# Optimization experiments

Measured on AMD Instinct MI355X. Metric: run time of the kernel, lower is better.

Reference implementation:

```python
import jax, jax.numpy as jnp
import numpy as np

N, E, De, Dv = 40000, 8000, 32, 8   # nodes, hyperedges, edge degree, node degree
D, Q, EIG, VOC, NC = 256, 256, 64, 1000, 40  # vertex/edge dim, query dim, eig dim, centrality vocab, classes
LN_EPS = 1e-5


def _linear(x, W, b):
    return x @ W + b


def _layernorm(x, g, b):
    mu = jnp.mean(x, axis=-1, keepdims=True)
    var = jnp.mean(jnp.square(x - mu), axis=-1, keepdims=True)
    return (x - mu) * jax.lax.rsqrt(var + LN_EPS) * g + b


def setup_inputs() -> dict:
    key = jax.random.key(0)
    ks = iter(jax.random.split(key, 64))
    def nrm(shape, s=0.02):
        return (jax.random.normal(next(ks), shape, jnp.float32) * s).astype(jnp.float32)
    inp = {
        'vfeat': jax.random.normal(next(ks), (N, D), jnp.float32),
        'efeat': jax.random.normal(next(ks), (E, D), jnp.float32),
        'eign_vec': jax.random.normal(next(ks), (N, EIG), jnp.float32),
        'feat_v_gcn': jax.random.normal(next(ks), (N, D), jnp.float32),
        'cent1': jax.random.uniform(next(ks), (E, De), jnp.float32),
        'cent2': jax.random.uniform(next(ks), (N, Dv), jnp.float32),
        'cent_idx': jax.random.randint(next(ks), (N,), 0, VOC),
        'uniq_idx': jax.random.randint(next(ks), (N,), 0, VOC),
        'edge2node': jax.random.randint(next(ks), (E, De), 0, N),
        'node2edge': jax.random.randint(next(ks), (N, Dv), 0, E),
        # learned parameters (W: [in, out])
        'W_vtx': nrm((D, D)), 'b_vtx': jnp.zeros((D,), jnp.float32),
        'W_pe': nrm((EIG, D)), 'b_pe': jnp.zeros((D,), jnp.float32),
        'cs_emb': nrm((VOC, D)), 'un_emb': nrm((VOC, D)),
        'W_kv': nrm((D, Q)), 'b_kv': jnp.zeros((Q,), jnp.float32),
        'W_vv': nrm((D, D)), 'b_vv': jnp.zeros((D,), jnp.float32),
        'W_qe': nrm((D, Q)), 'b_qe': jnp.zeros((Q,), jnp.float32),
        'W_ke': nrm((D, Q)), 'b_ke': jnp.zeros((Q,), jnp.float32),
        'W_ve': nrm((D, D)), 'b_ve': jnp.zeros((D,), jnp.float32),
        'W_qv': nrm((D, Q)), 'b_qv': jnp.zeros((Q,), jnp.float32),
        'W_l1': nrm((D, Q)), 'b_l1': jnp.zeros((Q,), jnp.float32),
        'W_l2': nrm((Q, D)), 'b_l2': jnp.zeros((D,), jnp.float32),
        'W_l3': nrm((D, Q)), 'b_l3': jnp.zeros((Q,), jnp.float32),
        'W_l4': nrm((Q, D)), 'b_l4': jnp.zeros((D,), jnp.float32),
        'ln1_g': jnp.ones((D,), jnp.float32), 'ln1_b': jnp.zeros((D,), jnp.float32),
        'ln2_g': jnp.ones((D,), jnp.float32), 'ln2_b': jnp.zeros((D,), jnp.float32),
        'W_cls': nrm((D, NC)), 'b_cls': jnp.zeros((NC,), jnp.float32),
    }
    return inp


def _forward(vfeat, efeat, eign_vec, feat_v_gcn, cent1, cent2,
             W_vtx, b_vtx, W_pe, b_pe, cs_emb, un_emb,
             W_kv, b_kv, W_vv, b_vv, W_qe, b_qe, W_ke, b_ke, W_ve, b_ve, W_qv, b_qv,
             W_l1, b_l1, W_l2, b_l2, W_l3, b_l3, W_l4, b_l4,
             ln1_g, ln1_b, ln2_g, ln2_b, W_cls, b_cls,
             cent_idx, uniq_idx, edge2node, node2edge):
    scale = 1.0 / np.sqrt(float(W_kv.shape[1]))  # 1/sqrt(query_dim)
    # first_layer feature assembly: vtx_lin_1layer + PE + GCN + centrality/uniqueness embeddings
    feat_v = (_linear(vfeat, W_vtx, b_vtx) + _linear(eign_vec, W_pe, b_pe)
              + feat_v_gcn + cs_emb[cent_idx] + un_emb[uniq_idx])
    feat_e = efeat

    # ---- stage 1: hyperedges attend over member nodes ('in' etype) ----
    k_n = _linear(feat_v, W_kv, b_kv)              # [N,Q]
    v_n = _linear(feat_v, W_vv, b_vv)              # [N,D]
    q_e = _linear(feat_e, W_qe, b_qe)              # [E,Q]
    km = k_n[edge2node]                            # [E,De,Q]
    attn = jax.nn.leaky_relu(jnp.einsum('edq,eq->ed', km, q_e), 0.01) * scale
    score = jax.nn.softmax(attn + cent1, axis=1)   # centrality-biased softmax (k-core + clustering)
    h_e = jnp.einsum('ed,edc->ec', score, v_n[edge2node])  # [E,D]
    x_e = _layernorm(h_e + feat_e, ln1_g, ln1_b)
    f_e = _linear(jax.nn.relu(_linear(x_e, W_l1, b_l1)), W_l2, b_l2)
    feat_e = _layernorm(f_e + x_e, ln1_g, ln1_b)

    # ---- stage 2: nodes attend over incident hyperedges ('con' etype) ----
    k_e = _linear(feat_e, W_ke, b_ke)              # [E,Q]
    v_e = _linear(feat_e, W_ve, b_ve)              # [E,D]
    q_v = _linear(feat_v, W_qv, b_qv)              # [N,Q]
    km2 = k_e[node2edge]                           # [N,Dv,Q]
    attn2 = jax.nn.leaky_relu(jnp.einsum('ndq,nq->nd', km2, q_v), 0.01) * scale
    score2 = jax.nn.softmax(attn2 + cent2, axis=1)
    h_v = jnp.einsum('nd,ndc->nc', score2, v_e[node2edge])  # [N,D]
    x_v = _layernorm(h_v + feat_v, ln2_g, ln2_b)
    f_v = _linear(jax.nn.relu(_linear(x_v, W_l3, b_l3)), W_l4, b_l4)
    feat_v = _layernorm(f_v + x_v, ln2_g, ln2_b)

    # last_layer classification head (dropout is identity in eval)
    return _linear(feat_v, W_cls, b_cls)           # [N,NC]


def reference(vfeat, efeat, eign_vec, feat_v_gcn, cent1, cent2,
              cent_idx, uniq_idx, edge2node, node2edge,
              W_vtx, b_vtx, W_pe, b_pe, cs_emb, un_emb,
              W_kv, b_kv, W_vv, b_vv, W_qe, b_qe, W_ke, b_ke, W_ve, b_ve, W_qv, b_qv,
              W_l1, b_l1, W_l2, b_l2, W_l3, b_l3, W_l4, b_l4,
              ln1_g, ln1_b, ln2_g, ln2_b, W_cls, b_cls):
    return _forward(vfeat, efeat, eign_vec, feat_v_gcn, cent1, cent2,
                    W_vtx, b_vtx, W_pe, b_pe, cs_emb, un_emb,
                    W_kv, b_kv, W_vv, b_vv, W_qe, b_qe, W_ke, b_ke, W_ve, b_ve, W_qv, b_qv,
                    W_l1, b_l1, W_l2, b_l2, W_l3, b_l3, W_l4, b_l4,
                    ln1_g, ln1_b, ln2_g, ln2_b, W_cls, b_cls,
                    cent_idx, uniq_idx, edge2node, node2edge)
```

## Files before the change

kernel.cpp:

```cpp
#include <hip/hip_runtime.h>
#include <hip/hip_bf16.h>
#include <cstddef>

#define N_NODES 40000
#define N_EDGES 8000
#define DE 32
#define DV 8
#define DIM 256
#define QDIM 256
#define EIGD 64
#define NCLS 40
#define LN_EPS 1e-5f
#define ATT_SCALE 0.0625f

typedef unsigned short u16;
typedef unsigned int u32;
using i16x8 = __attribute__((ext_vector_type(8))) short;
using f32x4 = __attribute__((ext_vector_type(4))) float;

__device__ inline u16 f2b(float f) {
    union { float f; u32 u; } c; c.f = f;
    u32 u = c.u + 0x7FFF + ((c.u >> 16) & 1);
    return (u16)(u >> 16);
}
__device__ inline float b2f(u16 b) {
    union { u32 u; float f; } c; c.u = (u32)b << 16;
    return c.f;
}

__device__ inline void gload_lds16(const u16* g, u16* l) {
    __builtin_amdgcn_global_load_lds(
        (const __attribute__((address_space(1))) void*)g,
        (__attribute__((address_space(3))) void*)l, 16, 0, 0);
}

#define VMCNT5  asm volatile("s_waitcnt vmcnt(5)" ::: "memory")
#define VMCNT4  asm volatile("s_waitcnt vmcnt(4)" ::: "memory")
#define VMCNT0  asm volatile("s_waitcnt vmcnt(0)" ::: "memory")
#define LGKM0   asm volatile("s_waitcnt lgkmcnt(0)" ::: "memory")

__global__ __launch_bounds__(256) void prep_weights(
    const float* w0, const float* w1, const float* w2, const float* w3,
    const float* w4, const float* w5, const float* w6, const float* w7,
    const float* w8, const float* w9, const float* w10, const float* w11,
    const float* w12, u16* __restrict__ pool)
{
    const float* srcs[13] = {w0,w1,w2,w3,w4,w5,w6,w7,w8,w9,w10,w11,w12};
    const int Ks[13]  = {256,64,256,256,256,256,256,256,256,256,256,256,256};
    const int Nds[13] = {256,256,256,256,256,256,256,256,256,256,256,256,40};
    const int id = blockIdx.z;
    const float* W = srcs[id];
    u16* Wt = pool + (size_t)id * 65536;
    const int K = Ks[id], Nd = Nds[id];
    const int k0 = blockIdx.x * 32, n0 = blockIdx.y * 32;
    if (k0 >= K || n0 >= Nd) return;

    __shared__ float tile[32][33];
    const int x = threadIdx.x & 31, y4 = (threadIdx.x >> 5) * 4;
#pragma unroll
    for (int j = 0; j < 4; j++) {
        int k = k0 + y4 + j;
        tile[y4 + j][x] = (k < K && (n0 + x) < Nd) ? W[(size_t)k * Nd + n0 + x] : 0.f;
    }
    __syncthreads();
#pragma unroll
    for (int j = 0; j < 4; j++) {
        int n = n0 + y4 + j;
        if (n < Nd && (k0 + x) < K)
            Wt[(size_t)n * K + k0 + x] = f2b(tile[x][y4 + j]);
    }
}

template <int EPI, int AMODE>
__global__ __launch_bounds__(256, 4) void gemm256(
    const void* __restrict__ Av, const float* __restrict__ A2,
    const u16* __restrict__ Wt, const u16* __restrict__ Wt2,
    const float* __restrict__ bias0, const float* __restrict__ bias1,
    const float* __restrict__ bias2, const u16* __restrict__ resid,
    const float* __restrict__ gcn, const float* __restrict__ emb1,
    const float* __restrict__ emb2, const int* __restrict__ idx1,
    const int* __restrict__ idx2, const float* __restrict__ lng,
    const float* __restrict__ lnb,
    void* __restrict__ Cv, int M, int Nd, int nt)
{
    __shared__ u16 Asm[2][64 * 32];
    __shared__ u16 Bsm[2][256 * 32];
    const int t = threadIdx.x;
    const int lane = t & 63, w = t >> 6;
    const int row0 = blockIdx.y * 64, col0 = blockIdx.x * 256;

    f32x4 acc[4][4] = {};

    const int srow = lane >> 2;
    const int sblk = ((lane & 3) ^ ((lane >> 3) & 3)) * 8;
    const int fr = lane & 15, h = lane >> 4;
    const int rsw = (fr >> 1) & 3;
    const bool wactive = (EPI != 4) || (w == 0);

    auto stage = [&](int buf, int kt) {
        const int k0 = kt << 5;
        const bool tail = (AMODE == 2) && (k0 >= 256);
        if constexpr (AMODE == 0) {
            gload_lds16((const u16*)Av + (size_t)(row0 + w * 16 + srow) * 256 + k0 + sblk,
                        &Asm[buf][(w * 16) * 32]);
#pragma unroll
            for (int i = 0; i < 4; i++) {
                const int r = w * 64 + i * 16;
                int ng = col0 + r + srow; if (ng > Nd - 1) ng = Nd - 1;
                gload_lds16(Wt + (size_t)ng * 256 + k0 + sblk, &Bsm[buf][r * 32]);
            }
        } else {
            const float* ap = tail
                ? A2 + (size_t)(row0 + w * 16 + srow) * 64 + (k0 - 256) + sblk
                : (const float*)Av + (size_t)(row0 + w * 16 + srow) * 256 + k0 + sblk;
            float4 f0 = *(const float4*)ap;
            float4 f1 = *(const float4*)(ap + 4);
#pragma unroll
            for (int i = 0; i < 4; i++) {
                const int r = w * 64 + i * 16;
                int ng = col0 + r + srow; if (ng > Nd - 1) ng = Nd - 1;
                const u16* gp = tail ? Wt2 + (size_t)ng * 64 + (k0 - 256) + sblk
                                     : Wt + (size_t)ng * 256 + k0 + sblk;
                gload_lds16(gp, &Bsm[buf][r * 32]);
            }
            i16x8 v;
            v[0] = (short)f2b(f0.x); v[1] = (short)f2b(f0.y);
            v[2] = (short)f2b(f0.z); v[3] = (short)f2b(f0.w);
            v[4] = (short)f2b(f1.x); v[5] = (short)f2b(f1.y);
            v[6] = (short)f2b(f1.z); v[7] = (short)f2b(f1.w);
            *(i16x8*)&Asm[buf][(w * 16 + srow) * 32 + (lane & 3) * 8] = v;
        }
    };

    stage(0, 0);
    for (int kt = 0; kt < nt; ++kt) {
        const int cur = kt & 1;
        const bool more = (kt + 1 < nt);
        if (more) stage(cur ^ 1, kt + 1);
        if (more) {
            if constexpr (AMODE == 0) { VMCNT5; } else { VMCNT4; }
        } else { VMCNT0; }
        if constexpr (AMODE != 0) { LGKM0; }
        __builtin_amdgcn_s_barrier();

        i16x8 af[4], bfr[4];
        if (wactive) {
#pragma unroll
            for (int m = 0; m < 4; m++)
                af[m] = *(const i16x8*)&Asm[cur][(m * 16 + fr) * 32 + (h ^ rsw) * 8];
#pragma unroll
            for (int n = 0; n < 4; n++)
                bfr[n] = *(const i16x8*)&Bsm[cur][(w * 64 + n * 16 + fr) * 32 + (h ^ rsw) * 8];
        }
        LGKM0;
        __builtin_amdgcn_sched_barrier(0);
        __builtin_amdgcn_s_barrier();

        if (wactive) {
#pragma unroll
            for (int m = 0; m < 4; m++)
#pragma unroll
                for (int n = 0; n < 4; n++)
                    acc[m][n] = __builtin_amdgcn_mfma_f32_16x16x32_bf16(
                        af[m], bfr[n], acc[m][n], 0, 0, 0);
        }
    }

    if constexpr (EPI == 5) {
        float* redS = (float*)&Asm[0][0];
        float* redQ = redS + 256;
#pragma unroll
        for (int m = 0; m < 4; m++) {
#pragma unroll
            for (int j = 0; j < 4; j++) {
                const int grow = row0 + m * 16 + h * 4 + j;
                float s = 0.f, q = 0.f;
#pragma unroll
                for (int n = 0; n < 4; n++) {
                    const int gcol = w * 64 + n * 16 + fr;
                    float v = acc[m][n][j] + bias0[gcol] +
                              b2f(resid[(size_t)grow * 256 + gcol]);
                    acc[m][n][j] = v;
                    s += v; q += v * v;
                }
#pragma unroll
                for (int off = 1; off < 16; off <<= 1) {
                    s += __shfl_xor(s, off, 64);
                    q += __shfl_xor(q, off, 64);
                }
                if (fr == 0) {
                    redS[(m * 16 + h * 4 + j) * 4 + w] = s;
                    redQ[(m * 16 + h * 4 + j) * 4 + w] = q;
                }
            }
        }
        __syncthreads();
#pragma unroll
        for (int m = 0; m < 4; m++) {
#pragma unroll
            for (int j = 0; j < 4; j++) {
                const int r = m * 16 + h * 4 + j;
                const int grow = row0 + r;
                float4 s4 = *(const float4*)&redS[r * 4];
                float4 q4 = *(const float4*)&redQ[r * 4];
                float mu = (s4.x + s4.y + s4.z + s4.w) * (1.f / DIM);
                float var = (q4.x + q4.y + q4.z + q4.w) * (1.f / DIM) - mu * mu;
                float rr = rsqrtf(var + LN_EPS);
#pragma unroll
                for (int n = 0; n < 4; n++) {
                    const int gcol = w * 64 + n * 16 + fr;
                    float y = (acc[m][n][j] - mu) * rr * lng[gcol] + lnb[gcol];
                    ((u16*)Cv)[(size_t)grow * 256 + gcol] = f2b(y);
                }
            }
        }
    } else {
        if (!wactive) return;
        const float* bp = (blockIdx.x == 0) ? bias0
                        : ((blockIdx.x == 1) ? bias1 : bias2);
#pragma unroll
        for (int m = 0; m < 4; m++) {
#pragma unroll
            for (int j = 0; j < 4; j++) {
                const int grow = row0 + m * 16 + h * 4 + j;
                int i1 = 0, i2 = 0;
                if constexpr (EPI == 3) { i1 = idx1[grow]; i2 = idx2[grow]; }
#pragma unroll
                for (int n = 0; n < 4; n++) {
                    const int gcol = col0 + w * 64 + n * 16 + fr;
                    if (EPI == 4 && gcol >= Nd) continue;
                    float v;
                    if constexpr (EPI == 3) {
                        v = acc[m][n][j] + bias0[gcol] + bias1[gcol];
                        v += gcn[(size_t)grow * 256 + gcol];
                        v += emb1[(size_t)i1 * 256 + gcol];
                        v += emb2[(size_t)i2 * 256 + gcol];
                    } else {
                        v = acc[m][n][j] + bp[gcol - col0];
                    }
                    if constexpr (EPI == 1) v = fmaxf(v, 0.f);
                    if constexpr (EPI == 4)
                        ((float*)Cv)[(size_t)grow * Nd + gcol] = v;
                    else
                        ((u16*)Cv)[(size_t)grow * Nd + gcol] = f2b(v);
                }
            }
        }
    }
}

__global__ __launch_bounds__(256) void edge_attn(
    const u16* __restrict__ KVQn, const u16* __restrict__ QE,
    const float* __restrict__ efeat,
    const int* __restrict__ e2n, const float* __restrict__ cent1,
    const float* __restrict__ g, const float* __restrict__ bb,
    u16* __restrict__ XE)
{
    const int lane = threadIdx.x & 63, w = threadIdx.x >> 6;
    const int e = blockIdx.x * 4 + w;
    const int c4 = lane * 4;

    ushort4 q4 = *(const ushort4*)&QE[(size_t)e * QDIM + c4];
    const float q0 = b2f(q4.x), q1 = b2f(q4.y), q2 = b2f(q4.z), q3 = b2f(q4.w);

    int4 rv[8];
#pragma unroll
    for (int i = 0; i < 8; i++)
        rv[i] = *(const int4*)&e2n[(size_t)e * DE + i * 4];
    int rows[DE];
#pragma unroll
    for (int i = 0; i < 8; i++) {
        rows[i * 4 + 0] = rv[i].x; rows[i * 4 + 1] = rv[i].y;
        rows[i * 4 + 2] = rv[i].z; rows[i * 4 + 3] = rv[i].w;
    }

    float p[DE];
#pragma unroll
    for (int g0 = 0; g0 < DE; g0 += 16) {
        ushort4 k4[16];
#pragma unroll
        for (int j = 0; j < 16; j++)
            k4[j] = *(const ushort4*)&KVQn[(size_t)rows[g0 + j] * 768 + c4];
#pragma unroll
        for (int j = 0; j < 16; j++)
            p[g0 + j] = q0 * b2f(k4[j].x) + q1 * b2f(k4[j].y)
                      + q2 * b2f(k4[j].z) + q3 * b2f(k4[j].w);
    }
#pragma unroll
    for (int off = 32; off; off >>= 1)
#pragma unroll
        for (int d = 0; d < DE; d++)
            p[d] += __shfl_xor(p[d], off, 64);

    float4 cv[8];
#pragma unroll
    for (int i = 0; i < 8; i++)
        cv[i] = *(const float4*)&cent1[(size_t)e * DE + i * 4];
    float cent[DE];
#pragma unroll
    for (int i = 0; i < 8; i++) {
        cent[i * 4 + 0] = cv[i].x; cent[i * 4 + 1] = cv[i].y;
        cent[i * 4 + 2] = cv[i].z; cent[i * 4 + 3] = cv[i].w;
    }
#pragma unroll
    for (int d = 0; d < DE; d++)
        p[d] = (p[d] > 0.f ? p[d] : 0.01f * p[d]) * ATT_SCALE + cent[d];

    float mx = p[0];
#pragma unroll
    for (int d = 1; d < DE; d++) mx = fmaxf(mx, p[d]);
    float s = 0.f;
#pragma unroll
    for (int d = 0; d < DE; d++) { p[d] = __expf(p[d] - mx); s += p[d]; }
    const float inv = 1.f / s;
#pragma unroll
    for (int d = 0; d < DE; d++) p[d] *= inv;

    float a0 = 0.f, a1 = 0.f, a2 = 0.f, a3 = 0.f;
#pragma unroll
    for (int g0 = 0; g0 < DE; g0 += 16) {
        ushort4 v4[16];
#pragma unroll
        for (int j = 0; j < 16; j++)
            v4[j] = *(const ushort4*)&KVQn[(size_t)rows[g0 + j] * 768 + 256 + c4];
#pragma unroll
        for (int j = 0; j < 16; j++) {
            const float sd = p[g0 + j];
            a0 = fmaf(sd, b2f(v4[j].x), a0); a1 = fmaf(sd, b2f(v4[j].y), a1);
            a2 = fmaf(sd, b2f(v4[j].z), a2); a3 = fmaf(sd, b2f(v4[j].w), a3);
        }
    }
    float4 ef = *(const float4*)&efeat[(size_t)e * DIM + c4];
    float x0 = a0 + ef.x, x1 = a1 + ef.y, x2 = a2 + ef.z, x3 = a3 + ef.w;

    float mu = x0 + x1 + x2 + x3;
#pragma unroll
    for (int off = 32; off; off >>= 1) mu += __shfl_xor(mu, off, 64);
    mu *= (1.f / DIM);
    float d0 = x0 - mu, d1 = x1 - mu, d2 = x2 - mu, d3 = x3 - mu;
    float var = d0 * d0 + d1 * d1 + d2 * d2 + d3 * d3;
#pragma unroll
    for (int off = 32; off; off >>= 1) var += __shfl_xor(var, off, 64);
    var *= (1.f / DIM);
    float r = rsqrtf(var + LN_EPS);
    float4 gv = *(const float4*)&g[c4];
    float4 bv = *(const float4*)&bb[c4];
    ushort4 o;
    o.x = f2b(d0 * r * gv.x + bv.x); o.y = f2b(d1 * r * gv.y + bv.y);
    o.z = f2b(d2 * r * gv.z + bv.z); o.w = f2b(d3 * r * gv.w + bv.w);
    *(ushort4*)&XE[(size_t)e * DIM + c4] = o;
}

__global__ __launch_bounds__(256) void node_attn(
    const u16* __restrict__ KVe, const u16* __restrict__ KVQn,
    const u16* __restrict__ FV,
    const int* __restrict__ n2e, const float* __restrict__ cent2,
    const float* __restrict__ g, const float* __restrict__ bb,
    u16* __restrict__ XV)
{
    const int lane = threadIdx.x & 63, w = threadIdx.x >> 6;
    const int na = blockIdx.x * 8 + w * 2, nb = na + 1;
    const int c4 = lane * 4;

    ushort4 qa4 = *(const ushort4*)&KVQn[(size_t)na * 768 + 512 + c4];
    ushort4 qb4 = *(const ushort4*)&KVQn[(size_t)nb * 768 + 512 + c4];
    const float qa0 = b2f(qa4.x), qa1 = b2f(qa4.y), qa2 = b2f(qa4.z), qa3 = b2f(qa4.w);
    const float qb0 = b2f(qb4.x), qb1 = b2f(qb4.y), qb2 = b2f(qb4.z), qb3 = b2f(qb4.w);

    int4 r0 = *(const int4*)&n2e[(size_t)na * DV];
    int4 r1 = *(const int4*)&n2e[(size_t)na * DV + 4];
    int4 r2 = *(const int4*)&n2e[(size_t)nb * DV];
    int4 r3 = *(const int4*)&n2e[(size_t)nb * DV + 4];
    int rA[8] = {r0.x, r0.y, r0.z, r0.w, r1.x, r1.y, r1.z, r1.w};
    int rB[8] = {r2.x, r2.y, r2.z, r2.w, r3.x, r3.y, r3.z, r3.w};

    ushort4 kA[8], vA[8], kB[8], vB[8];
#pragma unroll
    for (int d = 0; d < DV; d++) {
        const u16* b = KVe + (size_t)rA[d] * 512 + c4;
        kA[d] = *(const ushort4*)b; vA[d] = *(const ushort4*)(b + 256);
    }
#pragma unroll
    for (int d = 0; d < DV; d++) {
        const u16* b = KVe + (size_t)rB[d] * 512 + c4;
        kB[d] = *(const ushort4*)b; vB[d] = *(const ushort4*)(b + 256);
    }

    float pA[8], pB[8];
#pragma unroll
    for (int d = 0; d < DV; d++) {
        pA[d] = qa0 * b2f(kA[d].x) + qa1 * b2f(kA[d].y)
              + qa2 * b2f(kA[d].z) + qa3 * b2f(kA[d].w);
        pB[d] = qb0 * b2f(kB[d].x) + qb1 * b2f(kB[d].y)
              + qb2 * b2f(kB[d].z) + qb3 * b2f(kB[d].w);
    }
#pragma unroll
    for (int off = 32; off; off >>= 1) {
#pragma unroll
        for (int d = 0; d < DV; d++) {
            pA[d] += __shfl_xor(pA[d], off, 64);
            pB[d] += __shfl_xor(pB[d], off, 64);
        }
    }
    float4 cA0 = *(const float4*)&cent2[(size_t)na * DV];
    float4 cA1 = *(const float4*)&cent2[(size_t)na * DV + 4];
    float4 cB0 = *(const float4*)&cent2[(size_t)nb * DV];
    float4 cB1 = *(const float4*)&cent2[(size_t)nb * DV + 4];
    float cA[8] = {cA0.x, cA0.y, cA0.z, cA0.w, cA1.x, cA1.y, cA1.z, cA1.w};
    float cB[8] = {cB0.x, cB0.y, cB0.z, cB0.w, cB1.x, cB1.y, cB1.z, cB1.w};
#pragma unroll
    for (int d = 0; d < DV; d++) {
        pA[d] = (pA[d] > 0.f ? pA[d] : 0.01f * pA[d]) * ATT_SCALE + cA[d];
        pB[d] = (pB[d] > 0.f ? pB[d] : 0.01f * pB[d]) * ATT_SCALE + cB[d];
    }
    float mA = pA[0], mB = pB[0];
#pragma unroll
    for (int d = 1; d < DV; d++) { mA = fmaxf(mA, pA[d]); mB = fmaxf(mB, pB[d]); }
    float sA = 0.f, sB = 0.f;
#pragma unroll
    for (int d = 0; d < DV; d++) {
        pA[d] = __expf(pA[d] - mA); sA += pA[d];
        pB[d] = __expf(pB[d] - mB); sB += pB[d];
    }
    const float iA = 1.f / sA, iB = 1.f / sB;

    float a0 = 0.f, a1 = 0.f, a2 = 0.f, a3 = 0.f;
    float b0 = 0.f, b1 = 0.f, b2 = 0.f, b3 = 0.f;
#pragma unroll
    for (int d = 0; d < DV; d++) {
        const float sa = pA[d] * iA, sb = pB[d] * iB;
        a0 = fmaf(sa, b2f(vA[d].x), a0); a1 = fmaf(sa, b2f(vA[d].y), a1);
        a2 = fmaf(sa, b2f(vA[d].z), a2); a3 = fmaf(sa, b2f(vA[d].w), a3);
        b0 = fmaf(sb, b2f(vB[d].x), b0); b1 = fmaf(sb, b2f(vB[d].y), b1);
        b2 = fmaf(sb, b2f(vB[d].z), b2); b3 = fmaf(sb, b2f(vB[d].w), b3);
    }
    ushort4 fa = *(const ushort4*)&FV[(size_t)na * DIM + c4];
    ushort4 fb = *(const ushort4*)&FV[(size_t)nb * DIM + c4];
    float xa0 = a0 + b2f(fa.x), xa1 = a1 + b2f(fa.y);
    float xa2 = a2 + b2f(fa.z), xa3 = a3 + b2f(fa.w);
    float xb0 = b0 + b2f(fb.x), xb1 = b1 + b2f(fb.y);
    float xb2 = b2 + b2f(fb.z), xb3 = b3 + b2f(fb.w);

    float muA = xa0 + xa1 + xa2 + xa3, muB = xb0 + xb1 + xb2 + xb3;
#pragma unroll
    for (int off = 32; off; off >>= 1) {
        muA += __shfl_xor(muA, off, 64);
        muB += __shfl_xor(muB, off, 64);
    }
    muA *= (1.f / DIM); muB *= (1.f / DIM);
    float da0 = xa0 - muA, da1 = xa1 - muA, da2 = xa2 - muA, da3 = xa3 - muA;
    float db0 = xb0 - muB, db1 = xb1 - muB, db2 = xb2 - muB, db3 = xb3 - muB;
    float vA_ = da0 * da0 + da1 * da1 + da2 * da2 + da3 * da3;
    float vB_ = db0 * db0 + db1 * db1 + db2 * db2 + db3 * db3;
#pragma unroll
    for (int off = 32; off; off >>= 1) {
        vA_ += __shfl_xor(vA_, off, 64);
        vB_ += __shfl_xor(vB_, off, 64);
    }
    const float rA_ = rsqrtf(vA_ * (1.f / DIM) + LN_EPS);
    const float rB_ = rsqrtf(vB_ * (1.f / DIM) + LN_EPS);
    float4 gv = *(const float4*)&g[c4];
    float4 bv = *(const float4*)&bb[c4];
    ushort4 oa, ob;
    oa.x = f2b(da0 * rA_ * gv.x + bv.x); oa.y = f2b(da1 * rA_ * gv.y + bv.y);
    oa.z = f2b(da2 * rA_ * gv.z + bv.z); oa.w = f2b(da3 * rA_ * gv.w + bv.w);
    ob.x = f2b(db0 * rB_ * gv.x + bv.x); ob.y = f2b(db1 * rB_ * gv.y + bv.y);
    ob.z = f2b(db2 * rB_ * gv.z + bv.z); ob.w = f2b(db3 * rB_ * gv.w + bv.w);
    *(ushort4*)&XV[(size_t)na * DIM + c4] = oa;
    *(ushort4*)&XV[(size_t)nb * DIM + c4] = ob;
}

extern "C" void kernel_launch(void* const* d_in, const int* in_sizes, int n_in,
                              void* d_out, int out_size, void* d_ws, size_t ws_size,
                              hipStream_t stream)
{
    const float* vfeat  = (const float*)d_in[0];
    const float* efeat  = (const float*)d_in[1];
    const float* eign   = (const float*)d_in[2];
    const float* gcn    = (const float*)d_in[3];
    const float* cent1  = (const float*)d_in[4];
    const float* cent2  = (const float*)d_in[5];
    const int*   cidx   = (const int*)d_in[6];
    const int*   uidx   = (const int*)d_in[7];
    const int*   e2n    = (const int*)d_in[8];
    const int*   n2e    = (const int*)d_in[9];
    const float* W_vtx  = (const float*)d_in[10]; const float* b_vtx = (const float*)d_in[11];
    const float* W_pe   = (const float*)d_in[12]; const float* b_pe  = (const float*)d_in[13];
    const float* cs_emb = (const float*)d_in[14]; const float* un_emb= (const float*)d_in[15];
    const float* W_kv   = (const float*)d_in[16]; const float* b_kv  = (const float*)d_in[17];
    const float* W_vv   = (const float*)d_in[18]; const float* b_vv  = (const float*)d_in[19];
    const float* W_qe   = (const float*)d_in[20]; const float* b_qe  = (const float*)d_in[21];
    const float* W_ke   = (const float*)d_in[22]; const float* b_ke  = (const float*)d_in[23];
    const float* W_ve   = (const float*)d_in[24]; const float* b_ve  = (const float*)d_in[25];
    const float* W_qv   = (const float*)d_in[26]; const float* b_qv  = (const float*)d_in[27];
    const float* W_l1   = (const float*)d_in[28]; const float* b_l1  = (const float*)d_in[29];
    const float* W_l2   = (const float*)d_in[30]; const float* b_l2  = (const float*)d_in[31];
    const float* W_l3   = (const float*)d_in[32]; const float* b_l3  = (const float*)d_in[33];
    const float* W_l4   = (const float*)d_in[34]; const float* b_l4  = (const float*)d_in[35];
    const float* ln1_g  = (const float*)d_in[36]; const float* ln1_b = (const float*)d_in[37];
    const float* ln2_g  = (const float*)d_in[38]; const float* ln2_b = (const float*)d_in[39];
    const float* W_cls  = (const float*)d_in[40]; const float* b_cls = (const float*)d_in[41];
    float* out = (float*)d_out;

    const size_t NE = (size_t)N_NODES * DIM;
    const size_t EE = (size_t)N_EDGES * DIM;
    u16* ws = (u16*)d_ws;
    u16* FVb  = ws;
    u16* KVQn = FVb + NE;
    u16* B2   = KVQn + 3 * NE;
    u16* T0   = B2 + NE;
    u16* QEb  = T0 + NE;
    u16* XE   = QEb + EE;
    u16* TE   = XE + EE;
    u16* FE   = TE + EE;
    u16* KVe  = FE + EE;
    u16* Wp   = KVe + 2 * EE;
    u16* Wt_vtx = Wp +  0 * 65536;
    u16* Wt_pe  = Wp +  1 * 65536;
    u16* Wt_kvq = Wp +  2 * 65536;
    u16* Wt_qe  = Wp +  5 * 65536;
    u16* Wt_kve = Wp +  6 * 65536;
    u16* Wt_l1  = Wp +  8 * 65536;
    u16* Wt_l2  = Wp +  9 * 65536;
    u16* Wt_l3  = Wp + 10 * 65536;
    u16* Wt_l4  = Wp + 11 * 65536;
    u16* Wt_cls = Wp + 12 * 65536;

    const dim3 blk(256);
    const dim3 gW(8, 8, 13);
    const dim3 gN1(1, N_NODES / 64);
    const dim3 gKVQ(3, N_NODES / 64);
    const dim3 gE1(1, N_EDGES / 64);
    const dim3 gKVe(2, N_EDGES / 64);

    prep_weights<<<gW, blk, 0, stream>>>(
        W_vtx, W_pe, W_kv, W_vv, W_qv, W_qe, W_ke, W_ve,
        W_l1, W_l2, W_l3, W_l4, W_cls, Wp);

    gemm256<3, 2><<<gN1, blk, 0, stream>>>(vfeat, eign, Wt_vtx, Wt_pe,
        b_vtx, b_pe, nullptr, nullptr, gcn, cs_emb, un_emb, cidx, uidx,
        nullptr, nullptr, FVb, N_NODES, 256, 10);

    gemm256<0, 0><<<gKVQ, blk, 0, stream>>>(FVb, nullptr, Wt_kvq, nullptr,
        b_kv, b_vv, b_qv, nullptr, nullptr, nullptr, nullptr, nullptr, nullptr,
        nullptr, nullptr, KVQn, N_NODES, 768, 8);
    gemm256<0, 1><<<gE1, blk, 0, stream>>>(efeat, nullptr, Wt_qe, nullptr,
        b_qe, nullptr, nullptr, nullptr, nullptr, nullptr, nullptr, nullptr, nullptr,
        nullptr, nullptr, QEb, N_EDGES, 256, 8);
    edge_attn<<<N_EDGES / 4, blk, 0, stream>>>(KVQn, QEb, efeat, e2n, cent1,
        ln1_g, ln1_b, XE);
    gemm256<1, 0><<<gE1, blk, 0, stream>>>(XE, nullptr, Wt_l1, nullptr,
        b_l1, nullptr, nullptr, nullptr, nullptr, nullptr, nullptr, nullptr, nullptr,
        nullptr, nullptr, TE, N_EDGES, 256, 8);
    gemm256<5, 0><<<gE1, blk, 0, stream>>>(TE, nullptr, Wt_l2, nullptr,
        b_l2, nullptr, nullptr, XE, nullptr, nullptr, nullptr, nullptr, nullptr,
        ln1_g, ln1_b, FE, N_EDGES, 256, 8);

    gemm256<0, 0><<<gKVe, blk, 0, stream>>>(FE, nullptr, Wt_kve, nullptr,
        b_ke, b_ve, nullptr, nullptr, nullptr, nullptr, nullptr, nullptr, nullptr,
        nullptr, nullptr, KVe, N_EDGES, 512, 8);
    node_attn<<<N_NODES / 8, blk, 0, stream>>>(KVe, KVQn, FVb, n2e, cent2,
        ln2_g, ln2_b, B2);
    gemm256<1, 0><<<gN1, blk, 0, stream>>>(B2, nullptr, Wt_l3, nullptr,
        b_l3, nullptr, nullptr, nullptr, nullptr, nullptr, nullptr, nullptr, nullptr,
        nullptr, nullptr, T0, N_NODES, 256, 8);
    gemm256<5, 0><<<gN1, blk, 0, stream>>>(T0, nullptr, Wt_l4, nullptr,
        b_l4, nullptr, nullptr, B2, nullptr, nullptr, nullptr, nullptr, nullptr,
        ln2_g, ln2_b, FVb, N_NODES, 256, 8);

    gemm256<4, 0><<<gN1, blk, 0, stream>>>(FVb, nullptr, Wt_cls, nullptr,
        b_cls, nullptr, nullptr, nullptr, nullptr, nullptr, nullptr, nullptr, nullptr,
        nullptr, nullptr, out, N_NODES, NCLS, 8);
}
```

Baseline: 264.0 us.

## Split GEMMs into narrow-tile and full-width kernels with triple-buffered pipelines

The single generic GEMM becomes two kernels. gemmN uses 64x128 tiles with a K step of 64 and a 2x2 wave layout, for the plain bias/relu GEMMs and the classifier. gemmW keeps full 256-wide rows for the LayerNorm and embedding epilogues. Both use three LDS buffers with prefetch two stages ahead and a compile-time trip count, and fp32 A loads are held in registers so the bf16 conversion overlaps the next load. The aim is more blocks per GEMM and better overlap of loads with MFMA, at the cost of more LDS, occupancy lowered to 2 blocks per CU, and waitcnt values that must be hand-tuned to stay correct.

```diff
diff --git a/kernel.cpp b/kernel.cpp
--- a/kernel.cpp
+++ b/kernel.cpp
@@ -34,8 +34,10 @@
         (__attribute__((address_space(3))) void*)l, 16, 0, 0);
 }
 
+#define VMCNT12 asm volatile("s_waitcnt vmcnt(12)" ::: "memory")
+#define VMCNT10 asm volatile("s_waitcnt vmcnt(10)" ::: "memory")
+#define VMCNT6  asm volatile("s_waitcnt vmcnt(6)" ::: "memory")
 #define VMCNT5  asm volatile("s_waitcnt vmcnt(5)" ::: "memory")
-#define VMCNT4  asm volatile("s_waitcnt vmcnt(4)" ::: "memory")
 #define VMCNT0  asm volatile("s_waitcnt vmcnt(0)" ::: "memory")
 #define LGKM0   asm volatile("s_waitcnt lgkmcnt(0)" ::: "memory")
 
@@ -71,23 +73,152 @@
     }
 }
 
-template <int EPI, int AMODE>
-__global__ __launch_bounds__(256, 4) void gemm256(
+template <int EPI, int AMODE, int NT>
+__global__ __launch_bounds__(256, 2) void gemmN(
+    const void* __restrict__ Av, const u16* __restrict__ Wt,
+    const float* __restrict__ bias0, const float* __restrict__ bias1,
+    const float* __restrict__ bias2,
+    void* __restrict__ Cv, int Nd)
+{
+    __shared__ u16 Asm[3][64 * 64];
+    __shared__ u16 Bsm[3][128 * 64];
+    const int t = threadIdx.x;
+    const int lane = t & 63, w = t >> 6;
+    const int wr = w >> 1, wc = w & 1;
+    const int row0 = blockIdx.y * 64, col0 = blockIdx.x * 128;
+
+    f32x4 acc[2][4] = {};
+
+    const int srow = lane >> 3;
+    const int sblk = ((lane & 7) ^ srow) * 8;
+    const int fr = lane & 15, h = lane >> 4;
+    const int lsw = fr & 7;
+
+    float4 farA[2][2][2];
+
+    auto stage_load = [&](int kt) {
+        const int buf = kt % 3;
+        const int k0 = kt << 6;
+        if constexpr (AMODE == 0) {
+#pragma unroll
+            for (int i = 0; i < 2; i++) {
+                const int r = w * 16 + i * 8;
+                gload_lds16((const u16*)Av + (size_t)(row0 + r + srow) * 256 + k0 + sblk,
+                            &Asm[buf][r * 64]);
+            }
+        } else {
+#pragma unroll
+            for (int i = 0; i < 2; i++) {
+                const int r = w * 16 + i * 8;
+                const float* ap = (const float*)Av + (size_t)(row0 + r + srow) * 256 + k0 + sblk;
+                farA[kt & 1][i][0] = *(const float4*)ap;
+                farA[kt & 1][i][1] = *(const float4*)(ap + 4);
+            }
+        }
+#pragma unroll
+        for (int i = 0; i < 4; i++) {
+            const int r = w * 32 + i * 8;
+            int ng = col0 + r + srow; if (ng > Nd - 1) ng = Nd - 1;
+            gload_lds16(Wt + (size_t)ng * 256 + k0 + sblk, &Bsm[buf][r * 64]);
+        }
+    };
+    auto stage_write = [&](int kt) {
+        const int buf = kt % 3;
+#pragma unroll
+        for (int i = 0; i < 2; i++) {
+            const int r = w * 16 + i * 8;
+            float4 f0 = farA[kt & 1][i][0], f1 = farA[kt & 1][i][1];
+            i16x8 v;
+            v[0] = (short)f2b(f0.x); v[1] = (short)f2b(f0.y);
+            v[2] = (short)f2b(f0.z); v[3] = (short)f2b(f0.w);
+            v[4] = (short)f2b(f1.x); v[5] = (short)f2b(f1.y);
+            v[6] = (short)f2b(f1.z); v[7] = (short)f2b(f1.w);
+            *(i16x8*)&Asm[buf][(r + srow) * 64 + (lane & 7) * 8] = v;
+        }
+    };
+
+    stage_load(0);
+    if (NT > 1) stage_load(1);
+    if constexpr (AMODE != 0) stage_write(0);
+
+#pragma unroll
+    for (int kt = 0; kt < NT; ++kt) {
+        const int buf = kt % 3;
+        if (kt + 2 < NT) stage_load(kt + 2);
+        if constexpr (AMODE != 0) {
+            if (kt + 1 < NT) stage_write(kt + 1);
+            else { VMCNT0; }
+        } else {
+            if (kt + 2 < NT) { VMCNT12; }
+            else if (kt + 1 < NT) { VMCNT6; }
+            else { VMCNT0; }
+        }
+        __builtin_amdgcn_s_barrier();
+
+        i16x8 af[2][2], bfr[2][4];
+#pragma unroll
+        for (int kk = 0; kk < 2; kk++) {
+#pragma unroll
+            for (int m = 0; m < 2; m++)
+                af[kk][m] = *(const i16x8*)&Asm[buf][(wr * 32 + m * 16 + fr) * 64 +
+                                                    ((kk * 4 + h) ^ lsw) * 8];
+#pragma unroll
+            for (int n = 0; n < 4; n++)
+                bfr[kk][n] = *(const i16x8*)&Bsm[buf][(wc * 64 + n * 16 + fr) * 64 +
+                                                     ((kk * 4 + h) ^ lsw) * 8];
+        }
+        LGKM0;
+        __builtin_amdgcn_sched_barrier(0);
+        __builtin_amdgcn_s_barrier();
+
+#pragma unroll
+        for (int kk = 0; kk < 2; kk++)
+#pragma unroll
+            for (int m = 0; m < 2; m++)
+#pragma unroll
+                for (int n = 0; n < 4; n++)
+                    acc[m][n] = __builtin_amdgcn_mfma_f32_16x16x32_bf16(
+                        af[kk][m], bfr[kk][n], acc[m][n], 0, 0, 0);
+    }
+
+    const int seg = (int)(blockIdx.x >> 1);
+    const float* bp = (seg == 0) ? bias0 : ((seg == 1) ? bias1 : bias2);
+#pragma unroll
+    for (int m = 0; m < 2; m++) {
+#pragma unroll
+        for (int j = 0; j < 4; j++) {
+            const int grow = row0 + wr * 32 + m * 16 + h * 4 + j;
+#pragma unroll
+            for (int n = 0; n < 4; n++) {
+                const int gcol = col0 + wc * 64 + n * 16 + fr;
+                if (EPI == 4 && gcol >= Nd) continue;
+                float v = acc[m][n][j] + bp[gcol & 255];
+                if constexpr (EPI == 1) v = fmaxf(v, 0.f);
+                if constexpr (EPI == 4)
+                    ((float*)Cv)[(size_t)grow * Nd + gcol] = v;
+                else
+                    ((u16*)Cv)[(size_t)grow * Nd + gcol] = f2b(v);
+            }
+        }
+    }
+}
+
+template <int EPI, int AMODE, int NT>
+__global__ __launch_bounds__(256, 2) void gemmW(
     const void* __restrict__ Av, const float* __restrict__ A2,
     const u16* __restrict__ Wt, const u16* __restrict__ Wt2,
     const float* __restrict__ bias0, const float* __restrict__ bias1,
-    const float* __restrict__ bias2, const u16* __restrict__ resid,
+    const u16* __restrict__ resid,
     const float* __restrict__ gcn, const float* __restrict__ emb1,
     const float* __restrict__ emb2, const int* __restrict__ idx1,
     const int* __restrict__ idx2, const float* __restrict__ lng,
-    const float* __restrict__ lnb,
-    void* __restrict__ Cv, int M, int Nd, int nt)
+    const float* __restrict__ lnb, u16* __restrict__ Cv)
 {
-    __shared__ u16 Asm[2][64 * 32];
-    __shared__ u16 Bsm[2][256 * 32];
+    __shared__ u16 Asm[3][64 * 32];
+    __shared__ u16 Bsm[3][256 * 32];
     const int t = threadIdx.x;
     const int lane = t & 63, w = t >> 6;
-    const int row0 = blockIdx.y * 64, col0 = blockIdx.x * 256;
+    const int row0 = blockIdx.y * 64;
 
     f32x4 acc[4][4] = {};
 
@@ -95,75 +226,77 @@
     const int sblk = ((lane & 3) ^ ((lane >> 3) & 3)) * 8;
     const int fr = lane & 15, h = lane >> 4;
     const int rsw = (fr >> 1) & 3;
-    const bool wactive = (EPI != 4) || (w == 0);
-
-    auto stage = [&](int buf, int kt) {
+
+    float4 farA[2][2];
+
+    auto stage_load = [&](int kt) {
+        const int buf = kt % 3;
         const int k0 = kt << 5;
         const bool tail = (AMODE == 2) && (k0 >= 256);
         if constexpr (AMODE == 0) {
             gload_lds16((const u16*)Av + (size_t)(row0 + w * 16 + srow) * 256 + k0 + sblk,
                         &Asm[buf][(w * 16) * 32]);
-#pragma unroll
-            for (int i = 0; i < 4; i++) {
-                const int r = w * 64 + i * 16;
-                int ng = col0 + r + srow; if (ng > Nd - 1) ng = Nd - 1;
-                gload_lds16(Wt + (size_t)ng * 256 + k0 + sblk, &Bsm[buf][r * 32]);
-            }
         } else {
             const float* ap = tail
                 ? A2 + (size_t)(row0 + w * 16 + srow) * 64 + (k0 - 256) + sblk
                 : (const float*)Av + (size_t)(row0 + w * 16 + srow) * 256 + k0 + sblk;
-            float4 f0 = *(const float4*)ap;
-            float4 f1 = *(const float4*)(ap + 4);
-#pragma unroll
-            for (int i = 0; i < 4; i++) {
-                const int r = w * 64 + i * 16;
-                int ng = col0 + r + srow; if (ng > Nd - 1) ng = Nd - 1;
-                const u16* gp = tail ? Wt2 + (size_t)ng * 64 + (k0 - 256) + sblk
-                                     : Wt + (size_t)ng * 256 + k0 + sblk;
-                gload_lds16(gp, &Bsm[buf][r * 32]);
-            }
-            i16x8 v;
-            v[0] = (short)f2b(f0.x); v[1] = (short)f2b(f0.y);
-            v[2] = (short)f2b(f0.z); v[3] = (short)f2b(f0.w);
-            v[4] = (short)f2b(f1.x); v[5] = (short)f2b(f1.y);
-            v[6] = (short)f2b(f1.z); v[7] = (short)f2b(f1.w);
-            *(i16x8*)&Asm[buf][(w * 16 + srow) * 32 + (lane & 3) * 8] = v;
+            farA[kt & 1][0] = *(const float4*)ap;
+            farA[kt & 1][1] = *(const float4*)(ap + 4);
+        }
+#pragma unroll
+        for (int i = 0; i < 4; i++) {
+            const int r = w * 64 + i * 16;
+            const u16* gp = tail ? Wt2 + (size_t)(r + srow) * 64 + (k0 - 256) + sblk
+                                 : Wt + (size_t)(r + srow) * 256 + k0 + sblk;
+            gload_lds16(gp, &Bsm[buf][r * 32]);
         }
     };
-
-    stage(0, 0);
-    for (int kt = 0; kt < nt; ++kt) {
-        const int cur = kt & 1;
-        const bool more = (kt + 1 < nt);
-        if (more) stage(cur ^ 1, kt + 1);
-        if (more) {
-            if constexpr (AMODE == 0) { VMCNT5; } else { VMCNT4; }
-        } else { VMCNT0; }
-        if constexpr (AMODE != 0) { LGKM0; }
+    auto stage_write = [&](int kt) {
+        const int buf = kt % 3;
+        float4 f0 = farA[kt & 1][0], f1 = farA[kt & 1][1];
+        i16x8 v;
+        v[0] = (short)f2b(f0.x); v[1] = (short)f2b(f0.y);
+        v[2] = (short)f2b(f0.z); v[3] = (short)f2b(f0.w);
+        v[4] = (short)f2b(f1.x); v[5] = (short)f2b(f1.y);
+        v[6] = (short)f2b(f1.z); v[7] = (short)f2b(f1.w);
+        *(i16x8*)&Asm[buf][(w * 16 + srow) * 32 + (lane & 3) * 8] = v;
+    };
+
+    stage_load(0);
+    if (NT > 1) stage_load(1);
+    if constexpr (AMODE != 0) stage_write(0);
+
+#pragma unroll
+    for (int kt = 0; kt < NT; ++kt) {
+        const int buf = kt % 3;
+        if (kt + 2 < NT) stage_load(kt + 2);
+        if constexpr (AMODE != 0) {
+            if (kt + 1 < NT) stage_write(kt + 1);
+            else { VMCNT0; }
+        } else {
+            if (kt + 2 < NT) { VMCNT10; }
+            else if (kt + 1 < NT) { VMCNT5; }
+            else { VMCNT0; }
+        }
         __builtin_amdgcn_s_barrier();
 
         i16x8 af[4], bfr[4];
-        if (wactive) {
-#pragma unroll
-            for (int m = 0; m < 4; m++)
-                af[m] = *(const i16x8*)&Asm[cur][(m * 16 + fr) * 32 + (h ^ rsw) * 8];
-#pragma unroll
-            for (int n = 0; n < 4; n++)
-                bfr[n] = *(const i16x8*)&Bsm[cur][(w * 64 + n * 16 + fr) * 32 + (h ^ rsw) * 8];
-        }
+#pragma unroll
+        for (int m = 0; m < 4; m++)
+            af[m] = *(const i16x8*)&Asm[buf][(m * 16 + fr) * 32 + (h ^ rsw) * 8];
+#pragma unroll
+        for (int n = 0; n < 4; n++)
+            bfr[n] = *(const i16x8*)&Bsm[buf][(w * 64 + n * 16 + fr) * 32 + (h ^ rsw) * 8];
         LGKM0;
         __builtin_amdgcn_sched_barrier(0);
         __builtin_amdgcn_s_barrier();
 
-        if (wactive) {
-#pragma unroll
-            for (int m = 0; m < 4; m++)
-#pragma unroll
-                for (int n = 0; n < 4; n++)
-                    acc[m][n] = __builtin_amdgcn_mfma_f32_16x16x32_bf16(
-                        af[m], bfr[n], acc[m][n], 0, 0, 0);
-        }
+#pragma unroll
+        for (int m = 0; m < 4; m++)
+#pragma unroll
+            for (int n = 0; n < 4; n++)
+                acc[m][n] = __builtin_amdgcn_mfma_f32_16x16x32_bf16(
+                    af[m], bfr[n], acc[m][n], 0, 0, 0);
     }
 
     if constexpr (EPI == 5) {
@@ -210,39 +343,25 @@
                 for (int n = 0; n < 4; n++) {
                     const int gcol = w * 64 + n * 16 + fr;
                     float y = (acc[m][n][j] - mu) * rr * lng[gcol] + lnb[gcol];
-                    ((u16*)Cv)[(size_t)grow * 256 + gcol] = f2b(y);
+                    Cv[(size_t)grow * 256 + gcol] = f2b(y);
                 }
             }
         }
     } else {
-        if (!wactive) return;
-        const float* bp = (blockIdx.x == 0) ? bias0
-                        : ((blockIdx.x == 1) ? bias1 : bias2);
 #pragma unroll
         for (int m = 0; m < 4; m++) {
 #pragma unroll
             for (int j = 0; j < 4; j++) {
                 const int grow = row0 + m * 16 + h * 4 + j;
-                int i1 = 0, i2 = 0;
-                if constexpr (EPI == 3) { i1 = idx1[grow]; i2 = idx2[grow]; }
+                const int i1 = idx1[grow], i2 = idx2[grow];
 #pragma unroll
                 for (int n = 0; n < 4; n++) {
-                    const int gcol = col0 + w * 64 + n * 16 + fr;
-                    if (EPI == 4 && gcol >= Nd) continue;
-                    float v;
-                    if constexpr (EPI == 3) {
-                        v = acc[m][n][j] + bias0[gcol] + bias1[gcol];
-                        v += gcn[(size_t)grow * 256 + gcol];
-                        v += emb1[(size_t)i1 * 256 + gcol];
-                        v += emb2[(size_t)i2 * 256 + gcol];
-                    } else {
-                        v = acc[m][n][j] + bp[gcol - col0];
-                    }
-                    if constexpr (EPI == 1) v = fmaxf(v, 0.f);
-                    if constexpr (EPI == 4)
-                        ((float*)Cv)[(size_t)grow * Nd + gcol] = v;
-                    else
-                        ((u16*)Cv)[(size_t)grow * Nd + gcol] = f2b(v);
+                    const int gcol = w * 64 + n * 16 + fr;
+                    float v = acc[m][n][j] + bias0[gcol] + bias1[gcol];
+                    v += gcn[(size_t)grow * 256 + gcol];
+                    v += emb1[(size_t)i1 * 256 + gcol];
+                    v += emb2[(size_t)i2 * 256 + gcol];
+                    Cv[(size_t)grow * 256 + gcol] = f2b(v);
                 }
             }
         }
@@ -528,47 +647,46 @@
 
     const dim3 blk(256);
     const dim3 gW(8, 8, 13);
-    const dim3 gN1(1, N_NODES / 64);
-    const dim3 gKVQ(3, N_NODES / 64);
-    const dim3 gE1(1, N_EDGES / 64);
-    const dim3 gKVe(2, N_EDGES / 64);
+    const dim3 gAsm(1, N_NODES / 64);
+    const dim3 gKVQ(6, N_NODES / 64);
+    const dim3 gQE(2, N_EDGES / 64);
+    const dim3 gL1(2, N_EDGES / 64);
+    const dim3 gLNE(1, N_EDGES / 64);
+    const dim3 gKVe(4, N_EDGES / 64);
+    const dim3 gL3(2, N_NODES / 64);
+    const dim3 gLNN(1, N_NODES / 64);
+    const dim3 gCl(1, N_NODES / 64);
 
     prep_weights<<<gW, blk, 0, stream>>>(
         W_vtx, W_pe, W_kv, W_vv, W_qv, W_qe, W_ke, W_ve,
         W_l1, W_l2, W_l3, W_l4, W_cls, Wp);
 
-    gemm256<3, 2><<<gN1, blk, 0, stream>>>(vfeat, eign, Wt_vtx, Wt_pe,
-        b_vtx, b_pe, nullptr, nullptr, gcn, cs_emb, un_emb, cidx, uidx,
-        nullptr, nullptr, FVb, N_NODES, 256, 10);
-
-    gemm256<0, 0><<<gKVQ, blk, 0, stream>>>(FVb, nullptr, Wt_kvq, nullptr,
-        b_kv, b_vv, b_qv, nullptr, nullptr, nullptr, nullptr, nullptr, nullptr,
-        nullptr, nullptr, KVQn, N_NODES, 768, 8);
-    gemm256<0, 1><<<gE1, blk, 0, stream>>>(efeat, nullptr, Wt_qe, nullptr,
-        b_qe, nullptr, nullptr, nullptr, nullptr, nullptr, nullptr, nullptr, nullptr,
-        nullptr, nullptr, QEb, N_EDGES, 256, 8);
+    gemmW<3, 2, 10><<<gAsm, blk, 0, stream>>>(vfeat, eign, Wt_vtx, Wt_pe,
+        b_vtx, b_pe, nullptr, gcn, cs_emb, un_emb, cidx, uidx,
+        nullptr, nullptr, FVb);
+
+    gemmN<0, 0, 4><<<gKVQ, blk, 0, stream>>>(FVb, Wt_kvq,
+        b_kv, b_vv, b_qv, KVQn, 768);
+    gemmN<0, 1, 4><<<gQE, blk, 0, stream>>>(efeat, Wt_qe,
+        b_qe, b_qe, b_qe, QEb, 256);
     edge_attn<<<N_EDGES / 4, blk, 0, stream>>>(KVQn, QEb, efeat, e2n, cent1,
         ln1_g, ln1_b, XE);
-    gemm256<1, 0><<<gE1, blk, 0, stream>>>(XE, nullptr, Wt_l1, nullptr,
-        b_l1, nullptr, nullptr, nullptr, nullptr, nullptr, nullptr, nullptr, nullptr,
-        nullptr, nullptr, TE, N_EDGES, 256, 8);
-    gemm256<5, 0><<<gE1, blk, 0, stream>>>(TE, nullptr, Wt_l2, nullptr,
-        b_l2, nullptr, nullptr, XE, nullptr, nullptr, nullptr, nullptr, nullptr,
-        ln1_g, ln1_b, FE, N_EDGES, 256, 8);
-
-    gemm256<0, 0><<<gKVe, blk, 0, stream>>>(FE, nullptr, Wt_kve, nullptr,
-        b_ke, b_ve, nullptr, nullptr, nullptr, nullptr, nullptr, nullptr, nullptr,
-        nullptr, nullptr, KVe, N_EDGES, 512, 8);
+    gemmN<1, 0, 4><<<gL1, blk, 0, stream>>>(XE, Wt_l1,
+        b_l1, b_l1, b_l1, TE, 256);
+    gemmW<5, 0, 8><<<gLNE, blk, 0, stream>>>(TE, nullptr, Wt_l2, nullptr,
+        b_l2, nullptr, XE, nullptr, nullptr, nullptr, nullptr, nullptr,
+        ln1_g, ln1_b, FE);
+
+    gemmN<0, 0, 4><<<gKVe, blk, 0, stream>>>(FE, Wt_kve,
+        b_ke, b_ve, b_ve, KVe, 512);
     node_attn<<<N_NODES / 8, blk, 0, stream>>>(KVe, KVQn, FVb, n2e, cent2,
         ln2_g, ln2_b, B2);
-    gemm256<1, 0><<<gN1, blk, 0, stream>>>(B2, nullptr, Wt_l3, nullptr,
-        b_l3, nullptr, nullptr, nullptr, nullptr, nullptr, nullptr, nullptr, nullptr,
-        nullptr, nullptr, T0, N_NODES, 256, 8);
-    gemm256<5, 0><<<gN1, blk, 0, stream>>>(T0, nullptr, Wt_l4, nullptr,
-        b_l4, nullptr, nullptr, B2, nullptr, nullptr, nullptr, nullptr, nullptr,
-        ln2_g, ln2_b, FVb, N_NODES, 256, 8);
-
-    gemm256<4, 0><<<gN1, blk, 0, stream>>>(FVb, nullptr, Wt_cls, nullptr,
-        b_cls, nullptr, nullptr, nullptr, nullptr, nullptr, nullptr, nullptr, nullptr,
-        nullptr, nullptr, out, N_NODES, NCLS, 8);
-}
+    gemmN<1, 0, 4><<<gL3, blk, 0, stream>>>(B2, Wt_l3,
+        b_l3, b_l3, b_l3, T0, 256);
+    gemmW<5, 0, 8><<<gLNN, blk, 0, stream>>>(T0, nullptr, Wt_l4, nullptr,
+        b_l4, nullptr, B2, nullptr, nullptr, nullptr, nullptr, nullptr,
+        ln2_g, ln2_b, FVb);
+
+    gemmN<4, 0, 4><<<gCl, blk, 0, stream>>>(FVb, Wt_cls,
+        b_cls, b_cls, b_cls, out, NCLS);
+}
```

Result: no change. 260.6 us (-1.3%).
